# Kernel tuning notes

Hardware: AMD Instinct MI355X
Metric: run time of the kernel (lower is better)

The kernel has to match this reference:

```python
import jax, jax.numpy as jnp
import numpy as np

N = 50000        # nodes
E = 800000       # edges (avg degree 16)
F_IN = 128       # in_channels
HID = 32         # hidden_channels per head
H = 8            # heads
DH = HID * H     # 256, concat dim
NC = {'TL': 12, 'YL': 30, 'TS': 60, 'TZ': 120}
NEG_SLOPE = 0.2  # PyG GATConv default


def setup_inputs() -> dict:
    key = jax.random.key(0)
    ks = jax.random.split(key, 40)
    rn = lambda k, s, sc=0.1: jax.random.normal(k, s, jnp.float32) * sc
    inp = {}
    inp['x'] = jax.random.normal(ks[0], (N, F_IN), jnp.float32)
    inp['edge_index'] = jax.random.randint(ks[1], (2, E), 0, N, dtype=jnp.int64)
    # conv1: in -> H x HID (concat)
    inp['W1'] = rn(ks[2], (F_IN, DH)); inp['a1s'] = rn(ks[3], (H, HID)); inp['a1d'] = rn(ks[4], (H, HID)); inp['b1'] = jnp.zeros((DH,), jnp.float32)
    # conv2: DH -> H x HID (concat)
    inp['W2'] = rn(ks[5], (DH, DH)); inp['a2s'] = rn(ks[6], (H, HID)); inp['a2d'] = rn(ks[7], (H, HID)); inp['b2'] = jnp.zeros((DH,), jnp.float32)
    # task heads: DH -> C, heads=1, concat=False
    i = 8
    for t, c in NC.items():
        inp['W_' + t] = rn(ks[i], (DH, c)); i += 1
        inp['as_' + t] = rn(ks[i], (1, c)); i += 1
        inp['ad_' + t] = rn(ks[i], (1, c)); i += 1
        inp['b_' + t] = jnp.zeros((c,), jnp.float32)
    return inp


def gat_conv(x, src, dst, W, a_s, a_d, b, concat):
    """PyG-style GATConv (eval mode, self-loops already in src/dst)."""
    n = x.shape[0]
    heads, out_ch = a_s.shape
    h = (x @ W).reshape(n, heads, out_ch)                 # [N,H,C]
    alpha_s = jnp.einsum('nhc,hc->nh', h, a_s)            # [N,H]
    alpha_d = jnp.einsum('nhc,hc->nh', h, a_d)
    e = jax.nn.leaky_relu(alpha_s[src] + alpha_d[dst], NEG_SLOPE)   # [E,H]
    # numerically-stable segment softmax over incoming edges of each dst
    m = jax.ops.segment_max(e, dst, num_segments=n)
    ex = jnp.exp(e - m[dst])
    denom = jax.ops.segment_sum(ex, dst, num_segments=n)
    alpha = ex / (denom[dst] + 1e-16)                     # [E,H]
    out = jax.ops.segment_sum(alpha[:, :, None] * h[src], dst, num_segments=n)  # [N,H,C]
    out = out.reshape(n, heads * out_ch) if concat else out.mean(axis=1)
    return out + b


def reference(x, edge_index, W1, a1s, a1d, b1, W2, a2s, a2d, b2,
              W_TL, as_TL, ad_TL, b_TL, W_YL, as_YL, ad_YL, b_YL,
              W_TS, as_TS, ad_TS, b_TS, W_TZ, as_TZ, ad_TZ, b_TZ):
    n = x.shape[0]
    loop = jnp.arange(n, dtype=edge_index.dtype)
    src = jnp.concatenate([edge_index[0], loop])
    dst = jnp.concatenate([edge_index[1], loop])
    h = jax.nn.elu(gat_conv(x, src, dst, W1, a1s, a1d, b1, True))
    h = gat_conv(h, src, dst, W2, a2s, a2d, b2, True)
    tl = jax.nn.log_softmax(gat_conv(h, src, dst, W_TL, as_TL, ad_TL, b_TL, False), axis=1)
    yl = jax.nn.log_softmax(gat_conv(h, src, dst, W_YL, as_YL, ad_YL, b_YL, False), axis=1)
    ts = jax.nn.log_softmax(gat_conv(h, src, dst, W_TS, as_TS, ad_TS, b_TS, False), axis=1)
    tz = jax.nn.log_softmax(gat_conv(h, src, dst, W_TZ, as_TZ, ad_TZ, b_TZ, False), axis=1)
    return (tl, yl, ts, tz)
```

## Files before the change

### kernel.cpp

```cpp
#include <hip/hip_runtime.h>
#include <math.h>


#define NEG_SLOPE 0.2f

typedef short s8v __attribute__((ext_vector_type(8)));
typedef short s4v __attribute__((ext_vector_type(4)));
typedef float f4v __attribute__((ext_vector_type(4)));

__device__ __forceinline__ short f2bf(float x) {
    unsigned u = __float_as_uint(x);
    u += 0x7fffu + ((u >> 16) & 1u);
    return (short)(u >> 16);
}
__device__ __forceinline__ float bf2f(short b) {
    return __uint_as_float(((unsigned)(unsigned short)b) << 16);
}
__device__ __forceinline__ void split2(float x, short& h, short& l) {
    h = f2bf(x);
    l = f2bf(x - bf2f(h));
}
__device__ __forceinline__ float4 bf4_to_f4(s4v v) {
    return make_float4(bf2f(v[0]), bf2f(v[1]), bf2f(v[2]), bf2f(v[3]));
}
__device__ __forceinline__ int rfl_clamp(int v) {
    int s = __builtin_amdgcn_readfirstlane(v);
    return s < 0 ? 0 : s;
}


__global__ void init_kernel(int* __restrict__ deg, int* __restrict__ cursor, int n) {
    int i = blockIdx.x * blockDim.x + threadIdx.x;
    if (i < n) { deg[i] = 1; cursor[i] = 0; }
}

__global__ void count_kernel(const int* __restrict__ dst, int* __restrict__ deg, int E) {
    int i = blockIdx.x * blockDim.x + threadIdx.x;
    if (i < E) atomicAdd(&deg[dst[i]], 1);
}

__global__ __launch_bounds__(1024) void scan_kernel(const int* __restrict__ deg,
                                                    int* __restrict__ rowstart, int n) {
    __shared__ int wsum[16];
    __shared__ int carry_sh;
    int lane = threadIdx.x & 63, wv = threadIdx.x >> 6;
    if (threadIdx.x == 0) { carry_sh = 0; rowstart[0] = 0; }
    __syncthreads();
    for (int base = 0; base < n; base += 8192) {
        int vals[8];
        int sum = 0;
        int i0 = base + threadIdx.x * 8;
        #pragma unroll
        for (int j = 0; j < 8; ++j) {
            int i = i0 + j;
            int v = (i < n) ? ((deg[i] + 3) & ~3) : 0;
            sum += v;
            vals[j] = sum;
        }
        int incl = sum;
        #pragma unroll
        for (int off = 1; off < 64; off <<= 1) {
            int t = __shfl_up(incl, off);
            if (lane >= off) incl += t;
        }
        if (lane == 63) wsum[wv] = incl;
        __syncthreads();
        if (wv == 0) {
            int s = (lane < 16) ? wsum[lane] : 0;
            #pragma unroll
            for (int off = 1; off < 16; off <<= 1) {
                int t = __shfl_up(s, off);
                if (lane >= off) s += t;
            }
            if (lane < 16) wsum[lane] = s;
        }
        __syncthreads();
        int wexcl = (wv == 0) ? 0 : wsum[wv - 1];
        int excl = carry_sh + wexcl + (incl - sum);
        #pragma unroll
        for (int j = 0; j < 8; ++j) {
            int i = i0 + j;
            if (i < n) rowstart[i + 1] = excl + vals[j];
        }
        __syncthreads();
        if (threadIdx.x == 0) carry_sh += wsum[15];
        __syncthreads();
    }
}

__global__ void scatter_kernel(const int* __restrict__ src, const int* __restrict__ dst,
                               const int* __restrict__ rowstart, int* __restrict__ cursor,
                               int* __restrict__ csr, int* __restrict__ csrd, int E, int n) {
    int i = blockIdx.x * blockDim.x + threadIdx.x;
    if (i >= E + n) return;
    int s, d;
    if (i < E) { s = src[i]; d = dst[i]; }
    else       { s = d = i - E; }
    int p = atomicAdd(&cursor[d], 1);
    int slot = rowstart[d] + p;
    csr[slot] = s;
    csrd[slot] = d;
}


__global__ void tobf_kernel(const float* __restrict__ A, short* __restrict__ Ah, int n4) {
    int i = blockIdx.x * blockDim.x + threadIdx.x;
    if (i >= n4) return;
    float4 v = ((const float4*)A)[i];
    s4v hv = {f2bf(v.x), f2bf(v.y), f2bf(v.z), f2bf(v.w)};
    ((s4v*)Ah)[i] = hv;
}

__global__ void split_bt_kernel(const float* __restrict__ B, short* __restrict__ Bh,
                                short* __restrict__ Bl, int K, int Nc, int kshift) {
    int idx = blockIdx.x * blockDim.x + threadIdx.x;
    if (idx >= Nc * K) return;
    int n = idx >> kshift;
    int k = idx & (K - 1);
    float v = B[(size_t)k * Nc + n];
    short h, l; split2(v, h, l);
    Bh[idx] = h;
    Bl[idx] = l;
}

__global__ void fold_alpha8_kernel(const float* __restrict__ W,
                                   const float* __restrict__ a_s, const float* __restrict__ a_d,
                                   short* __restrict__ Bth, short* __restrict__ Btl,
                                   int K, int Nfeat) {
    int idx = blockIdx.x * blockDim.x + threadIdx.x;
    if (idx >= K * 16) return;
    int j = idx / K, k = idx % K;
    int h = j & 7;
    const float* av = ((j < 8) ? a_s : a_d) + h * 32;
    const float* wp = W + (size_t)k * 256 + h * 32;
    float s = 0.f;
    #pragma unroll
    for (int c = 0; c < 32; ++c) s += wp[c] * av[c];
    short hi, lo; split2(s, hi, lo);
    size_t off = (size_t)(Nfeat + j) * K + k;
    Bth[off] = hi; Btl[off] = lo;
}

__global__ void fold_alpha4_kernel(const float* __restrict__ Wcat,
                                   const float* __restrict__ ascat, const float* __restrict__ adcat,
                                   short* __restrict__ Bth, short* __restrict__ Btl) {
    int idx = blockIdx.x * blockDim.x + threadIdx.x;
    if (idx >= 256 * 8) return;
    int j = idx >> 8, k = idx & 255;
    const int CO[4] = {0, 12, 42, 102};
    const int CL[4] = {12, 30, 60, 120};
    int t = j & 3;
    const float* av = ((j < 4) ? ascat : adcat) + CO[t];
    const float* wp = Wcat + (size_t)k * 222 + CO[t];
    float s = 0.f;
    for (int c = 0; c < CL[t]; ++c) s += wp[c] * av[c];
    short hi, lo; split2(s, hi, lo);
    size_t off = (size_t)(222 + j) * 256 + k;
    Bth[off] = hi; Btl[off] = lo;
}


#define MB 128
#define NB 64
#define KS 32

__global__ __launch_bounds__(256) void gemm_mfma_kernel(
        const short* __restrict__ Ah_g,
        const short* __restrict__ Bth_g, const short* __restrict__ Btl_g,
        short* __restrict__ Cb, int cb_stride,
        float* __restrict__ als, float* __restrict__ ald, int nsplit,
        int M, int K, int Nfeat, int NcExt) {
    __shared__ __align__(16) short Ah[MB][40];
    __shared__ __align__(16) short Bh[NB][40];
    __shared__ __align__(16) short Bl[NB][40];

    int t = threadIdx.x;
    int lane = t & 63, w = t >> 6;
    int quad = lane >> 4, l16 = lane & 15;
    int row0 = blockIdx.y * MB, col0 = blockIdx.x * NB;

    f4v acc[2][4];
    #pragma unroll
    for (int mt = 0; mt < 2; ++mt)
        #pragma unroll
        for (int nt = 0; nt < 4; ++nt)
            acc[mt][nt] = (f4v){0.f, 0.f, 0.f, 0.f};

    for (int k0 = 0; k0 < K; k0 += KS) {
        __syncthreads();
        #pragma unroll
        for (int i = 0; i < 2; ++i) {
            int u = i * 256 + t;
            int r = u >> 2, kk = (u & 3) * 8;
            int gr = row0 + r;
            s8v vh = {0, 0, 0, 0, 0, 0, 0, 0};
            if (gr < M) vh = *(const s8v*)(Ah_g + (size_t)gr * K + k0 + kk);
            *(s8v*)&Ah[r][kk] = vh;
        }
        {
            int n = t >> 2, kk = (t & 3) * 8;
            int gc = col0 + n;
            s8v vh = {0, 0, 0, 0, 0, 0, 0, 0};
            s8v vl = {0, 0, 0, 0, 0, 0, 0, 0};
            if (gc < NcExt) {
                vh = *(const s8v*)(Bth_g + (size_t)gc * K + k0 + kk);
                vl = *(const s8v*)(Btl_g + (size_t)gc * K + k0 + kk);
            }
            *(s8v*)&Bh[n][kk] = vh;
            *(s8v*)&Bl[n][kk] = vl;
        }
        __syncthreads();

        int kb = quad * 8;
        s8v a_f[2], b_h[4], b_l[4];
        #pragma unroll
        for (int mt = 0; mt < 2; ++mt) {
            int r = w * 32 + mt * 16 + l16;
            a_f[mt] = *(const s8v*)&Ah[r][kb];
        }
        #pragma unroll
        for (int nt = 0; nt < 4; ++nt) {
            int c = nt * 16 + l16;
            b_h[nt] = *(const s8v*)&Bh[c][kb];
            b_l[nt] = *(const s8v*)&Bl[c][kb];
        }
        #pragma unroll
        for (int mt = 0; mt < 2; ++mt)
            #pragma unroll
            for (int nt = 0; nt < 4; ++nt) {
                acc[mt][nt] = __builtin_amdgcn_mfma_f32_16x16x32_bf16(
                    a_f[mt], b_h[nt], acc[mt][nt], 0, 0, 0);
                acc[mt][nt] = __builtin_amdgcn_mfma_f32_16x16x32_bf16(
                    a_f[mt], b_l[nt], acc[mt][nt], 0, 0, 0);
            }
    }

    #pragma unroll
    for (int mt = 0; mt < 2; ++mt) {
        #pragma unroll
        for (int nt = 0; nt < 4; ++nt) {
            int gc = col0 + nt * 16 + l16;
            if (gc >= NcExt) continue;
            #pragma unroll
            for (int r = 0; r < 4; ++r) {
                int gr = row0 + w * 32 + mt * 16 + quad * 4 + r;
                if (gr >= M) continue;
                float v = acc[mt][nt][r];
                if (gc < Nfeat) {
                    Cb[(size_t)gr * cb_stride + gc] = f2bf(v);
                } else {
                    int j = gc - Nfeat;
                    if (j < nsplit)            als[(size_t)gr * nsplit + j] = v;
                    else if (j < 2 * nsplit)   ald[(size_t)gr * nsplit + (j - nsplit)] = v;
                }
            }
        }
    }
}


__global__ void ew8_kernel(const float* __restrict__ als, const float* __restrict__ ald,
                           const int* __restrict__ csr, const int* __restrict__ csrd,
                           float* __restrict__ ew, int M4) {
    int i = blockIdx.x * blockDim.x + threadIdx.x;
    if (i >= M4) return;
    int s = csr[i], d = csrd[i];
    float4* op = (float4*)(ew + (size_t)i * 8);
    if (s < 0) {
        op[0] = make_float4(0.f, 0.f, 0.f, 0.f);
        op[1] = make_float4(0.f, 0.f, 0.f, 0.f);
        return;
    }
    const float4* ap = (const float4*)(als + (size_t)s * 8);
    const float4* dp = (const float4*)(ald + (size_t)d * 8);
    float4 a0 = ap[0], a1 = ap[1];
    float4 d0 = dp[0], d1 = dp[1];
    float v[8] = {a0.x + d0.x, a0.y + d0.y, a0.z + d0.z, a0.w + d0.w,
                  a1.x + d1.x, a1.y + d1.y, a1.z + d1.z, a1.w + d1.w};
    float w[8];
    #pragma unroll
    for (int h = 0; h < 8; ++h) {
        float x = v[h];
        x = (x > 0.f) ? x : NEG_SLOPE * x;
        w[h] = __expf(x);
    }
    op[0] = make_float4(w[0], w[1], w[2], w[3]);
    op[1] = make_float4(w[4], w[5], w[6], w[7]);
}


__global__ __launch_bounds__(256) void gat_gather_kernel(
        const short* __restrict__ hb, const float* __restrict__ ew,
        const int* __restrict__ rowstart, const int* __restrict__ csr,
        const float* __restrict__ bias, short* __restrict__ oh, int n, int elu) {
    int wid  = blockIdx.x * 4 + (threadIdx.x >> 6);
    int lane = threadIdx.x & 63;
    if (wid >= n) return;
    int row = rowstart[wid];
    int pdeg = rowstart[wid + 1] - row;
    int hp = lane >> 3;
    int ch = lane * 4;
    const int* cp = csr + row;
    const float* wp = ew + (size_t)row * 8 + hp;

    float4 acc = {0.f, 0.f, 0.f, 0.f};
    float wsum = 0.f;
    for (int e = 0; e < pdeg; e += 4) {
        int4 sv = *(const int4*)(cp + e);
        int s0 = rfl_clamp(sv.x);
        int s1 = rfl_clamp(sv.y);
        int s2 = rfl_clamp(sv.z);
        int s3 = rfl_clamp(sv.w);
        float w0 = wp[(size_t)(e + 0) * 8];
        float w1 = wp[(size_t)(e + 1) * 8];
        float w2 = wp[(size_t)(e + 2) * 8];
        float w3 = wp[(size_t)(e + 3) * 8];
        float4 h0 = bf4_to_f4(*(const s4v*)(hb + (size_t)s0 * 256 + ch));
        float4 h1 = bf4_to_f4(*(const s4v*)(hb + (size_t)s1 * 256 + ch));
        float4 h2 = bf4_to_f4(*(const s4v*)(hb + (size_t)s2 * 256 + ch));
        float4 h3 = bf4_to_f4(*(const s4v*)(hb + (size_t)s3 * 256 + ch));
        acc.x += w0 * h0.x + w1 * h1.x + w2 * h2.x + w3 * h3.x;
        acc.y += w0 * h0.y + w1 * h1.y + w2 * h2.y + w3 * h3.y;
        acc.z += w0 * h0.z + w1 * h1.z + w2 * h2.z + w3 * h3.z;
        acc.w += w0 * h0.w + w1 * h1.w + w2 * h2.w + w3 * h3.w;
        wsum += (w0 + w1) + (w2 + w3);
    }
    float inv = 1.f / (wsum + 1e-16f);
    float4 b4 = *(const float4*)(bias + ch);
    float v[4] = {acc.x * inv + b4.x, acc.y * inv + b4.y,
                  acc.z * inv + b4.z, acc.w * inv + b4.w};
    if (elu) {
        #pragma unroll
        for (int j = 0; j < 4; ++j)
            v[j] = (v[j] > 0.f) ? v[j] : __expf(v[j]) - 1.f;
    }
    s4v hv = {f2bf(v[0]), f2bf(v[1]), f2bf(v[2]), f2bf(v[3])};
    *(s4v*)(oh + (size_t)wid * 256 + ch) = hv;
}


__global__ void pack_w_kernel(const float* __restrict__ wTL, const float* __restrict__ wYL,
                              const float* __restrict__ wTS, const float* __restrict__ wTZ,
                              const float* __restrict__ bTL, const float* __restrict__ bYL,
                              const float* __restrict__ bTS, const float* __restrict__ bTZ,
                              const float* __restrict__ asTL, const float* __restrict__ asYL,
                              const float* __restrict__ asTS, const float* __restrict__ asTZ,
                              const float* __restrict__ adTL, const float* __restrict__ adYL,
                              const float* __restrict__ adTS, const float* __restrict__ adTZ,
                              float* __restrict__ Wcat, float* __restrict__ bcat,
                              float* __restrict__ ascat, float* __restrict__ adcat) {
    int idx = blockIdx.x * blockDim.x + threadIdx.x;
    if (idx < 256 * 222) {
        int r = idx / 222, c = idx % 222;
        float v;
        if (c < 12)       v = wTL[r * 12 + c];
        else if (c < 42)  v = wYL[r * 30 + (c - 12)];
        else if (c < 102) v = wTS[r * 60 + (c - 42)];
        else              v = wTZ[r * 120 + (c - 102)];
        Wcat[idx] = v;
    }
    if (idx < 222) {
        bcat[idx]  = (idx < 12) ? bTL[idx] : (idx < 42) ? bYL[idx - 12]
                   : (idx < 102) ? bTS[idx - 42] : bTZ[idx - 102];
        ascat[idx] = (idx < 12) ? asTL[idx] : (idx < 42) ? asYL[idx - 12]
                   : (idx < 102) ? asTS[idx - 42] : asTZ[idx - 102];
        adcat[idx] = (idx < 12) ? adTL[idx] : (idx < 42) ? adYL[idx - 12]
                   : (idx < 102) ? adTS[idx - 42] : adTZ[idx - 102];
    }
}


__global__ void ew4_kernel(const float* __restrict__ ast, const float* __restrict__ adt,
                           const int* __restrict__ csr, const int* __restrict__ csrd,
                           float* __restrict__ ew, int M4) {
    int i = blockIdx.x * blockDim.x + threadIdx.x;
    if (i >= M4) return;
    int s = csr[i], d = csrd[i];
    if (s < 0) {
        *(float4*)(ew + (size_t)i * 4) = make_float4(0.f, 0.f, 0.f, 0.f);
        return;
    }
    float4 a = *(const float4*)(ast + (size_t)s * 4);
    float4 b = *(const float4*)(adt + (size_t)d * 4);
    float v[4] = {a.x + b.x, a.y + b.y, a.z + b.z, a.w + b.w};
    float w[4];
    #pragma unroll
    for (int t = 0; t < 4; ++t) {
        float x = v[t];
        x = (x > 0.f) ? x : NEG_SLOPE * x;
        w[t] = __expf(x);
    }
    *(float4*)(ew + (size_t)i * 4) = make_float4(w[0], w[1], w[2], w[3]);
}


__device__ __forceinline__ float sel4(int t, float v0, float v1, float v2, float v3) {
    return (t == 0) ? v0 : (t == 1) ? v1 : (t == 2) ? v2 : v3;
}
__device__ __forceinline__ int sel4i(int t, int v0, int v1, int v2, int v3) {
    return (t == 0) ? v0 : (t == 1) ? v1 : (t == 2) ? v2 : v3;
}

__global__ __launch_bounds__(256) void task_gather_ls_kernel(
        const short* __restrict__ htb, const float* __restrict__ ew,
        const int* __restrict__ rowstart, const int* __restrict__ csr,
        const float* __restrict__ bcat, float* __restrict__ out, int n) {
    int wid  = blockIdx.x * 4 + (threadIdx.x >> 6);
    int lane = threadIdx.x & 63;
    if (wid >= n) return;
    int row = rowstart[wid];
    int pdeg = rowstart[wid + 1] - row;
    int ch0 = lane * 4;

    bool valj[4]; bool lo_j[4];
    int t_lo, t_hi;
    {
        int tj0 = (ch0 >= 102) ? 3 : (ch0 >= 42) ? 2 : (ch0 >= 12) ? 1 : 0;
        int ch3 = ch0 + 3;
        int tj3 = (ch3 >= 102) ? 3 : (ch3 >= 42) ? 2 : (ch3 >= 12) ? 1 : 0;
        t_lo = tj0; t_hi = tj3;
        #pragma unroll
        for (int j = 0; j < 4; ++j) {
            int ch = ch0 + j;
            valj[j] = (ch < 222);
            int tj = (ch >= 102) ? 3 : (ch >= 42) ? 2 : (ch >= 12) ? 1 : 0;
            lo_j[j] = (tj == t_lo);
        }
    }

    const int* cp = csr + row;
    const float* wp = ew + (size_t)row * 4;

    float acc[4] = {0.f, 0.f, 0.f, 0.f};
    float ws_lo = 0.f, ws_hi = 0.f;
    for (int e = 0; e < pdeg; e += 4) {
        int4 sv = *(const int4*)(cp + e);
        int s0 = rfl_clamp(sv.x);
        int s1 = rfl_clamp(sv.y);
        int s2 = rfl_clamp(sv.z);
        int s3 = rfl_clamp(sv.w);
        float wlo0 = wp[(size_t)(e + 0) * 4 + t_lo], whi0 = wp[(size_t)(e + 0) * 4 + t_hi];
        float wlo1 = wp[(size_t)(e + 1) * 4 + t_lo], whi1 = wp[(size_t)(e + 1) * 4 + t_hi];
        float wlo2 = wp[(size_t)(e + 2) * 4 + t_lo], whi2 = wp[(size_t)(e + 2) * 4 + t_hi];
        float wlo3 = wp[(size_t)(e + 3) * 4 + t_lo], whi3 = wp[(size_t)(e + 3) * 4 + t_hi];
        float4 h0 = bf4_to_f4(*(const s4v*)(htb + (size_t)s0 * 224 + ch0));
        float4 h1 = bf4_to_f4(*(const s4v*)(htb + (size_t)s1 * 224 + ch0));
        float4 h2 = bf4_to_f4(*(const s4v*)(htb + (size_t)s2 * 224 + ch0));
        float4 h3 = bf4_to_f4(*(const s4v*)(htb + (size_t)s3 * 224 + ch0));
        ws_lo += (wlo0 + wlo1) + (wlo2 + wlo3);
        ws_hi += (whi0 + whi1) + (whi2 + whi3);
        float hv0[4] = {h0.x, h0.y, h0.z, h0.w};
        float hv1[4] = {h1.x, h1.y, h1.z, h1.w};
        float hv2[4] = {h2.x, h2.y, h2.z, h2.w};
        float hv3[4] = {h3.x, h3.y, h3.z, h3.w};
        #pragma unroll
        for (int j = 0; j < 4; ++j) {
            float w0 = lo_j[j] ? wlo0 : whi0;
            float w1 = lo_j[j] ? wlo1 : whi1;
            float w2 = lo_j[j] ? wlo2 : whi2;
            float w3 = lo_j[j] ? wlo3 : whi3;
            acc[j] += w0 * hv0[j] + w1 * hv1[j] + w2 * hv2[j] + w3 * hv3[j];
        }
    }
    float inv_lo = 1.f / (ws_lo + 1e-16f);
    float inv_hi = 1.f / (ws_hi + 1e-16f);

    float vout[4];
    float m_lo = -1e30f, m_hi = -1e30f;
    #pragma unroll
    for (int j = 0; j < 4; ++j) {
        float v = 0.f;
        if (valj[j]) {
            v = acc[j] * (lo_j[j] ? inv_lo : inv_hi) + bcat[ch0 + j];
            if (lo_j[j]) m_lo = fmaxf(m_lo, v); else m_hi = fmaxf(m_hi, v);
        }
        vout[j] = v;
    }
    float m0 = -1e30f, m1 = -1e30f, m2 = -1e30f, m3 = -1e30f;
    m0 = (t_lo == 0) ? fmaxf(m0, m_lo) : m0;  m0 = (t_hi == 0) ? fmaxf(m0, m_hi) : m0;
    m1 = (t_lo == 1) ? fmaxf(m1, m_lo) : m1;  m1 = (t_hi == 1) ? fmaxf(m1, m_hi) : m1;
    m2 = (t_lo == 2) ? fmaxf(m2, m_lo) : m2;  m2 = (t_hi == 2) ? fmaxf(m2, m_hi) : m2;
    m3 = (t_lo == 3) ? fmaxf(m3, m_lo) : m3;  m3 = (t_hi == 3) ? fmaxf(m3, m_hi) : m3;
    #pragma unroll
    for (int off = 1; off < 64; off <<= 1) {
        m0 = fmaxf(m0, __shfl_xor(m0, off));
        m1 = fmaxf(m1, __shfl_xor(m1, off));
        m2 = fmaxf(m2, __shfl_xor(m2, off));
        m3 = fmaxf(m3, __shfl_xor(m3, off));
    }
    float mt_lo = sel4(t_lo, m0, m1, m2, m3);
    float mt_hi = sel4(t_hi, m0, m1, m2, m3);
    float s_lo = 0.f, s_hi = 0.f;
    #pragma unroll
    for (int j = 0; j < 4; ++j) {
        if (valj[j]) {
            if (lo_j[j]) s_lo += __expf(vout[j] - mt_lo);
            else         s_hi += __expf(vout[j] - mt_hi);
        }
    }
    float s0 = ((t_lo == 0) ? s_lo : 0.f) + ((t_hi == 0 && t_hi != t_lo) ? s_hi : 0.f);
    float s1 = ((t_lo == 1) ? s_lo : 0.f) + ((t_hi == 1 && t_hi != t_lo) ? s_hi : 0.f);
    float s2 = ((t_lo == 2) ? s_lo : 0.f) + ((t_hi == 2 && t_hi != t_lo) ? s_hi : 0.f);
    float s3 = ((t_lo == 3) ? s_lo : 0.f) + ((t_hi == 3 && t_hi != t_lo) ? s_hi : 0.f);
    #pragma unroll
    for (int off = 1; off < 64; off <<= 1) {
        s0 += __shfl_xor(s0, off);
        s1 += __shfl_xor(s1, off);
        s2 += __shfl_xor(s2, off);
        s3 += __shfl_xor(s3, off);
    }
    float l0 = m0 + __logf(s0), l1 = m1 + __logf(s1);
    float l2 = m2 + __logf(s2), l3 = m3 + __logf(s3);
    float lse_lo = sel4(t_lo, l0, l1, l2, l3);
    float lse_hi = sel4(t_hi, l0, l1, l2, l3);
    int co_lo = sel4i(t_lo, 0, 12, 42, 102), cl_lo = sel4i(t_lo, 12, 30, 60, 120);
    int co_hi = sel4i(t_hi, 0, 12, 42, 102), cl_hi = sel4i(t_hi, 12, 30, 60, 120);
    #pragma unroll
    for (int j = 0; j < 4; ++j) {
        if (!valj[j]) continue;
        int co = lo_j[j] ? co_lo : co_hi;
        int cl = lo_j[j] ? cl_lo : cl_hi;
        float lse = lo_j[j] ? lse_lo : lse_hi;
        out[(size_t)co * n + (size_t)wid * cl + (ch0 + j - co)] = vout[j] - lse;
    }
}


extern "C" void kernel_launch(void* const* d_in, const int* in_sizes, int n_in,
                              void* d_out, int out_size, void* d_ws, size_t ws_size,
                              hipStream_t stream) {
    const float* x   = (const float*)d_in[0];
    const int*   ei  = (const int*)d_in[1];
    const float* W1  = (const float*)d_in[2];
    const float* a1s = (const float*)d_in[3];
    const float* a1d = (const float*)d_in[4];
    const float* b1  = (const float*)d_in[5];
    const float* W2  = (const float*)d_in[6];
    const float* a2s = (const float*)d_in[7];
    const float* a2d = (const float*)d_in[8];
    const float* b2  = (const float*)d_in[9];
    const float* W_TL = (const float*)d_in[10]; const float* as_TL = (const float*)d_in[11];
    const float* ad_TL = (const float*)d_in[12]; const float* b_TL = (const float*)d_in[13];
    const float* W_YL = (const float*)d_in[14]; const float* as_YL = (const float*)d_in[15];
    const float* ad_YL = (const float*)d_in[16]; const float* b_YL = (const float*)d_in[17];
    const float* W_TS = (const float*)d_in[18]; const float* as_TS = (const float*)d_in[19];
    const float* ad_TS = (const float*)d_in[20]; const float* b_TS = (const float*)d_in[21];
    const float* W_TZ = (const float*)d_in[22]; const float* as_TZ = (const float*)d_in[23];
    const float* ad_TZ = (const float*)d_in[24]; const float* b_TZ = (const float*)d_in[25];

    const int N = in_sizes[0] / 128;
    const int E = in_sizes[1] / 2;
    const int* e_src = ei;
    const int* e_dst = ei + E;
    const int M4 = E + 4 * N;

    float* ws = (float*)d_ws;
    float* B1   = ws;
    float* B2   = B1 + (size_t)N * 256;
    float* B3   = B2 + (size_t)N * 256;
    float* as1  = B3 + (size_t)N * 256;
    float* ad1  = as1 + (size_t)N * 8;
    float* as2  = ad1 + (size_t)N * 8;
    float* ad2  = as2 + (size_t)N * 8;
    float* ast  = ad2 + (size_t)N * 8;
    float* adt  = ast + (size_t)N * 4;
    float* Wcat = adt + (size_t)N * 4;
    float* bcat = Wcat + 256 * 222;
    float* ascat = bcat + 224;
    float* adcat = ascat + 224;
    int* deg      = (int*)(adcat + 224);
    int* rowstart = deg + N;
    int* cursor   = rowstart + (N + 4);
    int* csr      = cursor + N;
    int* csrd     = csr + M4;
    uintptr_t wsp = (uintptr_t)(csrd + M4);
    wsp = (wsp + 15) & ~(uintptr_t)15;
    short* W1h = (short*)wsp;
    short* W1l = W1h + 272 * 128;
    short* W2h = W1l + 272 * 128;
    short* W2l = W2h + 272 * 256;
    short* Wth = W2l + 272 * 256;
    short* Wtl = Wth + 230 * 256;
    short* Xh  = (short*)B1;
    short* Sh  = (short*)B1;
    short* Th  = (short*)B1;
    short* h1b = (short*)B2;
    short* h2b = (short*)B2;
    short* htb = (short*)B2;
    float* ew1 = B3;
    float* ew2 = B3;
    float* ewt = B3;

    float* out = (float*)d_out;

    const int B = 256;
    init_kernel<<<(N + B - 1) / B, B, 0, stream>>>(deg, cursor, N);
    count_kernel<<<(E + B - 1) / B, B, 0, stream>>>(e_dst, deg, E);
    scan_kernel<<<1, 1024, 0, stream>>>(deg, rowstart, N);
    hipMemsetAsync(csr, 0xFF, (size_t)2 * M4 * sizeof(int), stream);
    scatter_kernel<<<(E + N + B - 1) / B, B, 0, stream>>>(e_src, e_dst, rowstart, cursor, csr, csrd, E, N);
    pack_w_kernel<<<(256 * 222 + B - 1) / B, B, 0, stream>>>(W_TL, W_YL, W_TS, W_TZ,
        b_TL, b_YL, b_TS, b_TZ, as_TL, as_YL, as_TS, as_TZ, ad_TL, ad_YL, ad_TS, ad_TZ,
        Wcat, bcat, ascat, adcat);
    split_bt_kernel<<<(256 * 128 + B - 1) / B, B, 0, stream>>>(W1, W1h, W1l, 128, 256, 7);
    split_bt_kernel<<<(256 * 256 + B - 1) / B, B, 0, stream>>>(W2, W2h, W2l, 256, 256, 8);
    split_bt_kernel<<<(222 * 256 + B - 1) / B, B, 0, stream>>>(Wcat, Wth, Wtl, 256, 222, 8);
    fold_alpha8_kernel<<<(128 * 16 + B - 1) / B, B, 0, stream>>>(W1, a1s, a1d, W1h, W1l, 128, 256);
    fold_alpha8_kernel<<<(256 * 16 + B - 1) / B, B, 0, stream>>>(W2, a2s, a2d, W2h, W2l, 256, 256);
    fold_alpha4_kernel<<<(256 * 8 + B - 1) / B, B, 0, stream>>>(Wcat, ascat, adcat, Wth, Wtl);
    tobf_kernel<<<((N * 128 / 4) + B - 1) / B, B, 0, stream>>>(x, Xh, N * 128 / 4);
    {
        dim3 g((272 + NB - 1) / NB, (N + MB - 1) / MB);
        gemm_mfma_kernel<<<g, 256, 0, stream>>>(Xh, W1h, W1l, h1b, 256,
                                                as1, ad1, 8, N, 128, 256, 272);
    }
    ew8_kernel<<<(M4 + B - 1) / B, B, 0, stream>>>(as1, ad1, csr, csrd, ew1, M4);
    gat_gather_kernel<<<(N + 3) / 4, 256, 0, stream>>>(h1b, ew1, rowstart, csr, b1, Sh, N, 1);
    {
        dim3 g((272 + NB - 1) / NB, (N + MB - 1) / MB);
        gemm_mfma_kernel<<<g, 256, 0, stream>>>(Sh, W2h, W2l, h2b, 256,
                                                as2, ad2, 8, N, 256, 256, 272);
    }
    ew8_kernel<<<(M4 + B - 1) / B, B, 0, stream>>>(as2, ad2, csr, csrd, ew2, M4);
    gat_gather_kernel<<<(N + 3) / 4, 256, 0, stream>>>(h2b, ew2, rowstart, csr, b2, Th, N, 0);
    {
        dim3 g((230 + NB - 1) / NB, (N + MB - 1) / MB);
        gemm_mfma_kernel<<<g, 256, 0, stream>>>(Th, Wth, Wtl, htb, 224,
                                                ast, adt, 4, N, 256, 222, 230);
    }
    ew4_kernel<<<(M4 + B - 1) / B, B, 0, stream>>>(ast, adt, csr, csrd, ewt, M4);
    task_gather_ls_kernel<<<(N + 3) / 4, 256, 0, stream>>>(htb, ewt, rowstart, csr, bcat, out, N);
}
```

Before: 631.3 us.

## Transpose edge weights to head-major, batch index loads via readlane in gathers

Edge attention weights are stored head-major ([H][M4]) instead of edge-major, so each lane reads contiguous float4 weights for a run of edges. The gather kernels load up to 64 CSR indices once per wave and broadcast them with readlane, unrolling by 8 to put more independent row loads in flight. The task-head columns are padded so each lane's 4 channels fall in a single task, which simplifies the log-softmax logic. The cost is strided writes in the ew kernels and slightly wider task GEMM output.

```diff
diff --git a/kernel.cpp b/kernel.cpp
--- a/kernel.cpp
+++ b/kernel.cpp
@@ -23,8 +23,8 @@
 __device__ __forceinline__ float4 bf4_to_f4(s4v v) {
     return make_float4(bf2f(v[0]), bf2f(v[1]), bf2f(v[2]), bf2f(v[3]));
 }
-__device__ __forceinline__ int rfl_clamp(int v) {
-    int s = __builtin_amdgcn_readfirstlane(v);
+__device__ __forceinline__ int rl_at(int v, int e) {
+    int s = __builtin_amdgcn_readlane(v, e);
     return s < 0 ? 0 : s;
 }
 
@@ -147,15 +147,15 @@
     int idx = blockIdx.x * blockDim.x + threadIdx.x;
     if (idx >= 256 * 8) return;
     int j = idx >> 8, k = idx & 255;
-    const int CO[4] = {0, 12, 42, 102};
-    const int CL[4] = {12, 30, 60, 120};
+    const int CO[4] = {0, 12, 44, 104};
+    const int CL[4] = {12, 32, 60, 120};
     int t = j & 3;
     const float* av = ((j < 4) ? ascat : adcat) + CO[t];
-    const float* wp = Wcat + (size_t)k * 222 + CO[t];
+    const float* wp = Wcat + (size_t)k * 224 + CO[t];
     float s = 0.f;
     for (int c = 0; c < CL[t]; ++c) s += wp[c] * av[c];
     short hi, lo; split2(s, hi, lo);
-    size_t off = (size_t)(222 + j) * 256 + k;
+    size_t off = (size_t)(224 + j) * 256 + k;
     Bth[off] = hi; Btl[off] = lo;
 }
 
@@ -261,14 +261,13 @@
 
 __global__ void ew8_kernel(const float* __restrict__ als, const float* __restrict__ ald,
                            const int* __restrict__ csr, const int* __restrict__ csrd,
-                           float* __restrict__ ew, int M4) {
+                           float* __restrict__ ewT, int M4) {
     int i = blockIdx.x * blockDim.x + threadIdx.x;
     if (i >= M4) return;
     int s = csr[i], d = csrd[i];
-    float4* op = (float4*)(ew + (size_t)i * 8);
     if (s < 0) {
-        op[0] = make_float4(0.f, 0.f, 0.f, 0.f);
-        op[1] = make_float4(0.f, 0.f, 0.f, 0.f);
+        #pragma unroll
+        for (int h = 0; h < 8; ++h) ewT[(size_t)h * M4 + i] = 0.f;
         return;
     }
     const float4* ap = (const float4*)(als + (size_t)s * 8);
@@ -277,22 +276,20 @@
     float4 d0 = dp[0], d1 = dp[1];
     float v[8] = {a0.x + d0.x, a0.y + d0.y, a0.z + d0.z, a0.w + d0.w,
                   a1.x + d1.x, a1.y + d1.y, a1.z + d1.z, a1.w + d1.w};
-    float w[8];
     #pragma unroll
     for (int h = 0; h < 8; ++h) {
         float x = v[h];
         x = (x > 0.f) ? x : NEG_SLOPE * x;
-        w[h] = __expf(x);
-    }
-    op[0] = make_float4(w[0], w[1], w[2], w[3]);
-    op[1] = make_float4(w[4], w[5], w[6], w[7]);
+        ewT[(size_t)h * M4 + i] = __expf(x);
+    }
 }
 
 
 __global__ __launch_bounds__(256) void gat_gather_kernel(
-        const short* __restrict__ hb, const float* __restrict__ ew,
+        const short* __restrict__ hb, const float* __restrict__ ewT,
         const int* __restrict__ rowstart, const int* __restrict__ csr,
-        const float* __restrict__ bias, short* __restrict__ oh, int n, int elu) {
+        const float* __restrict__ bias, short* __restrict__ oh, int n, int elu,
+        int M4) {
     int wid  = blockIdx.x * 4 + (threadIdx.x >> 6);
     int lane = threadIdx.x & 63;
     if (wid >= n) return;
@@ -301,29 +298,53 @@
     int hp = lane >> 3;
     int ch = lane * 4;
     const int* cp = csr + row;
-    const float* wp = ew + (size_t)row * 8 + hp;
+    const float* wp = ewT + (size_t)hp * M4 + row;
 
     float4 acc = {0.f, 0.f, 0.f, 0.f};
     float wsum = 0.f;
-    for (int e = 0; e < pdeg; e += 4) {
-        int4 sv = *(const int4*)(cp + e);
-        int s0 = rfl_clamp(sv.x);
-        int s1 = rfl_clamp(sv.y);
-        int s2 = rfl_clamp(sv.z);
-        int s3 = rfl_clamp(sv.w);
-        float w0 = wp[(size_t)(e + 0) * 8];
-        float w1 = wp[(size_t)(e + 1) * 8];
-        float w2 = wp[(size_t)(e + 2) * 8];
-        float w3 = wp[(size_t)(e + 3) * 8];
-        float4 h0 = bf4_to_f4(*(const s4v*)(hb + (size_t)s0 * 256 + ch));
-        float4 h1 = bf4_to_f4(*(const s4v*)(hb + (size_t)s1 * 256 + ch));
-        float4 h2 = bf4_to_f4(*(const s4v*)(hb + (size_t)s2 * 256 + ch));
-        float4 h3 = bf4_to_f4(*(const s4v*)(hb + (size_t)s3 * 256 + ch));
-        acc.x += w0 * h0.x + w1 * h1.x + w2 * h2.x + w3 * h3.x;
-        acc.y += w0 * h0.y + w1 * h1.y + w2 * h2.y + w3 * h3.y;
-        acc.z += w0 * h0.z + w1 * h1.z + w2 * h2.z + w3 * h3.z;
-        acc.w += w0 * h0.w + w1 * h1.w + w2 * h2.w + w3 * h3.w;
-        wsum += (w0 + w1) + (w2 + w3);
+    for (int base = 0; base < pdeg; base += 64) {
+        int cnt = min(pdeg - base, 64);
+        int idxv = -1;
+        if (lane < cnt) idxv = cp[base + lane];
+        const float* wpb = wp + base;
+        int e = 0;
+        for (; e + 8 <= cnt; e += 8) {
+            int si[8];
+            #pragma unroll
+            for (int i = 0; i < 8; ++i) si[i] = rl_at(idxv, e + i);
+            float4 wa = *(const float4*)(wpb + e);
+            float4 wb = *(const float4*)(wpb + e + 4);
+            s4v hv[8];
+            #pragma unroll
+            for (int i = 0; i < 8; ++i)
+                hv[i] = *(const s4v*)(hb + (size_t)si[i] * 256 + ch);
+            float wv[8] = {wa.x, wa.y, wa.z, wa.w, wb.x, wb.y, wb.z, wb.w};
+            #pragma unroll
+            for (int i = 0; i < 8; ++i) {
+                float4 h = bf4_to_f4(hv[i]);
+                acc.x += wv[i] * h.x; acc.y += wv[i] * h.y;
+                acc.z += wv[i] * h.z; acc.w += wv[i] * h.w;
+                wsum += wv[i];
+            }
+        }
+        for (; e < cnt; e += 4) {
+            int si[4];
+            #pragma unroll
+            for (int i = 0; i < 4; ++i) si[i] = rl_at(idxv, e + i);
+            float4 wa = *(const float4*)(wpb + e);
+            s4v hv[4];
+            #pragma unroll
+            for (int i = 0; i < 4; ++i)
+                hv[i] = *(const s4v*)(hb + (size_t)si[i] * 256 + ch);
+            float wv[4] = {wa.x, wa.y, wa.z, wa.w};
+            #pragma unroll
+            for (int i = 0; i < 4; ++i) {
+                float4 h = bf4_to_f4(hv[i]);
+                acc.x += wv[i] * h.x; acc.y += wv[i] * h.y;
+                acc.z += wv[i] * h.z; acc.w += wv[i] * h.w;
+                wsum += wv[i];
+            }
+        }
     }
     float inv = 1.f / (wsum + 1e-16f);
     float4 b4 = *(const float4*)(bias + ch);
@@ -334,8 +355,8 @@
         for (int j = 0; j < 4; ++j)
             v[j] = (v[j] > 0.f) ? v[j] : __expf(v[j]) - 1.f;
     }
-    s4v hv = {f2bf(v[0]), f2bf(v[1]), f2bf(v[2]), f2bf(v[3])};
-    *(s4v*)(oh + (size_t)wid * 256 + ch) = hv;
+    s4v hvo = {f2bf(v[0]), f2bf(v[1]), f2bf(v[2]), f2bf(v[3])};
+    *(s4v*)(oh + (size_t)wid * 256 + ch) = hvo;
 }
 
 
@@ -350,137 +371,139 @@
                               float* __restrict__ Wcat, float* __restrict__ bcat,
                               float* __restrict__ ascat, float* __restrict__ adcat) {
     int idx = blockIdx.x * blockDim.x + threadIdx.x;
-    if (idx < 256 * 222) {
-        int r = idx / 222, c = idx % 222;
-        float v;
+    if (idx < 256 * 224) {
+        int r = idx / 224, c = idx % 224;
+        float v = 0.f;
         if (c < 12)       v = wTL[r * 12 + c];
         else if (c < 42)  v = wYL[r * 30 + (c - 12)];
-        else if (c < 102) v = wTS[r * 60 + (c - 42)];
-        else              v = wTZ[r * 120 + (c - 102)];
+        else if (c < 44)  v = 0.f;
+        else if (c < 104) v = wTS[r * 60 + (c - 44)];
+        else              v = wTZ[r * 120 + (c - 104)];
         Wcat[idx] = v;
     }
-    if (idx < 222) {
-        bcat[idx]  = (idx < 12) ? bTL[idx] : (idx < 42) ? bYL[idx - 12]
-                   : (idx < 102) ? bTS[idx - 42] : bTZ[idx - 102];
-        ascat[idx] = (idx < 12) ? asTL[idx] : (idx < 42) ? asYL[idx - 12]
-                   : (idx < 102) ? asTS[idx - 42] : asTZ[idx - 102];
-        adcat[idx] = (idx < 12) ? adTL[idx] : (idx < 42) ? adYL[idx - 12]
-                   : (idx < 102) ? adTS[idx - 42] : adTZ[idx - 102];
+    if (idx < 224) {
+        float b = 0.f, as_ = 0.f, ad_ = 0.f;
+        if (idx < 12)       { b = bTL[idx];       as_ = asTL[idx];       ad_ = adTL[idx]; }
+        else if (idx < 42)  { b = bYL[idx - 12];  as_ = asYL[idx - 12];  ad_ = adYL[idx - 12]; }
+        else if (idx < 44)  { }
+        else if (idx < 104) { b = bTS[idx - 44];  as_ = asTS[idx - 44];  ad_ = adTS[idx - 44]; }
+        else                { b = bTZ[idx - 104]; as_ = asTZ[idx - 104]; ad_ = adTZ[idx - 104]; }
+        bcat[idx]  = b;
+        ascat[idx] = as_;
+        adcat[idx] = ad_;
     }
 }
 
 
 __global__ void ew4_kernel(const float* __restrict__ ast, const float* __restrict__ adt,
                            const int* __restrict__ csr, const int* __restrict__ csrd,
-                           float* __restrict__ ew, int M4) {
+                           float* __restrict__ ewT, int M4) {
     int i = blockIdx.x * blockDim.x + threadIdx.x;
     if (i >= M4) return;
     int s = csr[i], d = csrd[i];
     if (s < 0) {
-        *(float4*)(ew + (size_t)i * 4) = make_float4(0.f, 0.f, 0.f, 0.f);
+        #pragma unroll
+        for (int t = 0; t < 4; ++t) ewT[(size_t)t * M4 + i] = 0.f;
         return;
     }
     float4 a = *(const float4*)(ast + (size_t)s * 4);
     float4 b = *(const float4*)(adt + (size_t)d * 4);
     float v[4] = {a.x + b.x, a.y + b.y, a.z + b.z, a.w + b.w};
-    float w[4];
     #pragma unroll
     for (int t = 0; t < 4; ++t) {
         float x = v[t];
         x = (x > 0.f) ? x : NEG_SLOPE * x;
-        w[t] = __expf(x);
-    }
-    *(float4*)(ew + (size_t)i * 4) = make_float4(w[0], w[1], w[2], w[3]);
+        ewT[(size_t)t * M4 + i] = __expf(x);
+    }
 }
 
 
 __device__ __forceinline__ float sel4(int t, float v0, float v1, float v2, float v3) {
     return (t == 0) ? v0 : (t == 1) ? v1 : (t == 2) ? v2 : v3;
 }
-__device__ __forceinline__ int sel4i(int t, int v0, int v1, int v2, int v3) {
-    return (t == 0) ? v0 : (t == 1) ? v1 : (t == 2) ? v2 : v3;
-}
 
 __global__ __launch_bounds__(256) void task_gather_ls_kernel(
-        const short* __restrict__ htb, const float* __restrict__ ew,
+        const short* __restrict__ htb, const float* __restrict__ ewT,
         const int* __restrict__ rowstart, const int* __restrict__ csr,
-        const float* __restrict__ bcat, float* __restrict__ out, int n) {
+        const float* __restrict__ bcat, float* __restrict__ out, int n, int M4) {
     int wid  = blockIdx.x * 4 + (threadIdx.x >> 6);
     int lane = threadIdx.x & 63;
     if (wid >= n) return;
     int row = rowstart[wid];
     int pdeg = rowstart[wid + 1] - row;
     int ch0 = lane * 4;
-
-    bool valj[4]; bool lo_j[4];
-    int t_lo, t_hi;
-    {
-        int tj0 = (ch0 >= 102) ? 3 : (ch0 >= 42) ? 2 : (ch0 >= 12) ? 1 : 0;
-        int ch3 = ch0 + 3;
-        int tj3 = (ch3 >= 102) ? 3 : (ch3 >= 42) ? 2 : (ch3 >= 12) ? 1 : 0;
-        t_lo = tj0; t_hi = tj3;
-        #pragma unroll
-        for (int j = 0; j < 4; ++j) {
-            int ch = ch0 + j;
-            valj[j] = (ch < 222);
-            int tj = (ch >= 102) ? 3 : (ch >= 42) ? 2 : (ch >= 12) ? 1 : 0;
-            lo_j[j] = (tj == t_lo);
-        }
-    }
+    int t = (lane < 3) ? 0 : (lane < 11) ? 1 : (lane < 26) ? 2 : 3;
+    int COp = (t == 0) ? 0 : (t == 1) ? 12 : (t == 2) ? 44 : 104;
+    int COr = (t == 0) ? 0 : (t == 1) ? 12 : (t == 2) ? 42 : 102;
+    int CLr = (t == 0) ? 12 : (t == 1) ? 30 : (t == 2) ? 60 : 120;
+    bool valj[4];
+    #pragma unroll
+    for (int j = 0; j < 4; ++j)
+        valj[j] = (unsigned)(ch0 + j - COp) < (unsigned)CLr;
 
     const int* cp = csr + row;
-    const float* wp = ew + (size_t)row * 4;
+    const float* wp = ewT + (size_t)t * M4 + row;
 
     float acc[4] = {0.f, 0.f, 0.f, 0.f};
-    float ws_lo = 0.f, ws_hi = 0.f;
-    for (int e = 0; e < pdeg; e += 4) {
-        int4 sv = *(const int4*)(cp + e);
-        int s0 = rfl_clamp(sv.x);
-        int s1 = rfl_clamp(sv.y);
-        int s2 = rfl_clamp(sv.z);
-        int s3 = rfl_clamp(sv.w);
-        float wlo0 = wp[(size_t)(e + 0) * 4 + t_lo], whi0 = wp[(size_t)(e + 0) * 4 + t_hi];
-        float wlo1 = wp[(size_t)(e + 1) * 4 + t_lo], whi1 = wp[(size_t)(e + 1) * 4 + t_hi];
-        float wlo2 = wp[(size_t)(e + 2) * 4 + t_lo], whi2 = wp[(size_t)(e + 2) * 4 + t_hi];
-        float wlo3 = wp[(size_t)(e + 3) * 4 + t_lo], whi3 = wp[(size_t)(e + 3) * 4 + t_hi];
-        float4 h0 = bf4_to_f4(*(const s4v*)(htb + (size_t)s0 * 224 + ch0));
-        float4 h1 = bf4_to_f4(*(const s4v*)(htb + (size_t)s1 * 224 + ch0));
-        float4 h2 = bf4_to_f4(*(const s4v*)(htb + (size_t)s2 * 224 + ch0));
-        float4 h3 = bf4_to_f4(*(const s4v*)(htb + (size_t)s3 * 224 + ch0));
-        ws_lo += (wlo0 + wlo1) + (wlo2 + wlo3);
-        ws_hi += (whi0 + whi1) + (whi2 + whi3);
-        float hv0[4] = {h0.x, h0.y, h0.z, h0.w};
-        float hv1[4] = {h1.x, h1.y, h1.z, h1.w};
-        float hv2[4] = {h2.x, h2.y, h2.z, h2.w};
-        float hv3[4] = {h3.x, h3.y, h3.z, h3.w};
-        #pragma unroll
-        for (int j = 0; j < 4; ++j) {
-            float w0 = lo_j[j] ? wlo0 : whi0;
-            float w1 = lo_j[j] ? wlo1 : whi1;
-            float w2 = lo_j[j] ? wlo2 : whi2;
-            float w3 = lo_j[j] ? wlo3 : whi3;
-            acc[j] += w0 * hv0[j] + w1 * hv1[j] + w2 * hv2[j] + w3 * hv3[j];
-        }
-    }
-    float inv_lo = 1.f / (ws_lo + 1e-16f);
-    float inv_hi = 1.f / (ws_hi + 1e-16f);
+    float ws = 0.f;
+    for (int base = 0; base < pdeg; base += 64) {
+        int cnt = min(pdeg - base, 64);
+        int idxv = -1;
+        if (lane < cnt) idxv = cp[base + lane];
+        const float* wpb = wp + base;
+        int e = 0;
+        for (; e + 8 <= cnt; e += 8) {
+            int si[8];
+            #pragma unroll
+            for (int i = 0; i < 8; ++i) si[i] = rl_at(idxv, e + i);
+            float4 wa = *(const float4*)(wpb + e);
+            float4 wb = *(const float4*)(wpb + e + 4);
+            s4v hv[8];
+            #pragma unroll
+            for (int i = 0; i < 8; ++i)
+                hv[i] = *(const s4v*)(htb + (size_t)si[i] * 224 + ch0);
+            float wv[8] = {wa.x, wa.y, wa.z, wa.w, wb.x, wb.y, wb.z, wb.w};
+            #pragma unroll
+            for (int i = 0; i < 8; ++i) {
+                float4 h = bf4_to_f4(hv[i]);
+                acc[0] += wv[i] * h.x; acc[1] += wv[i] * h.y;
+                acc[2] += wv[i] * h.z; acc[3] += wv[i] * h.w;
+                ws += wv[i];
+            }
+        }
+        for (; e < cnt; e += 4) {
+            int si[4];
+            #pragma unroll
+            for (int i = 0; i < 4; ++i) si[i] = rl_at(idxv, e + i);
+            float4 wa = *(const float4*)(wpb + e);
+            s4v hv[4];
+            #pragma unroll
+            for (int i = 0; i < 4; ++i)
+                hv[i] = *(const s4v*)(htb + (size_t)si[i] * 224 + ch0);
+            float wv[4] = {wa.x, wa.y, wa.z, wa.w};
+            #pragma unroll
+            for (int i = 0; i < 4; ++i) {
+                float4 h = bf4_to_f4(hv[i]);
+                acc[0] += wv[i] * h.x; acc[1] += wv[i] * h.y;
+                acc[2] += wv[i] * h.z; acc[3] += wv[i] * h.w;
+                ws += wv[i];
+            }
+        }
+    }
+    float inv = 1.f / (ws + 1e-16f);
 
     float vout[4];
-    float m_lo = -1e30f, m_hi = -1e30f;
+    float m = -1e30f;
     #pragma unroll
     for (int j = 0; j < 4; ++j) {
         float v = 0.f;
-        if (valj[j]) {
-            v = acc[j] * (lo_j[j] ? inv_lo : inv_hi) + bcat[ch0 + j];
-            if (lo_j[j]) m_lo = fmaxf(m_lo, v); else m_hi = fmaxf(m_hi, v);
-        }
+        if (valj[j]) { v = acc[j] * inv + bcat[ch0 + j]; m = fmaxf(m, v); }
         vout[j] = v;
     }
-    float m0 = -1e30f, m1 = -1e30f, m2 = -1e30f, m3 = -1e30f;
-    m0 = (t_lo == 0) ? fmaxf(m0, m_lo) : m0;  m0 = (t_hi == 0) ? fmaxf(m0, m_hi) : m0;
-    m1 = (t_lo == 1) ? fmaxf(m1, m_lo) : m1;  m1 = (t_hi == 1) ? fmaxf(m1, m_hi) : m1;
-    m2 = (t_lo == 2) ? fmaxf(m2, m_lo) : m2;  m2 = (t_hi == 2) ? fmaxf(m2, m_hi) : m2;
-    m3 = (t_lo == 3) ? fmaxf(m3, m_lo) : m3;  m3 = (t_hi == 3) ? fmaxf(m3, m_hi) : m3;
+    float m0 = (t == 0) ? m : -1e30f;
+    float m1 = (t == 1) ? m : -1e30f;
+    float m2 = (t == 2) ? m : -1e30f;
+    float m3 = (t == 3) ? m : -1e30f;
     #pragma unroll
     for (int off = 1; off < 64; off <<= 1) {
         m0 = fmaxf(m0, __shfl_xor(m0, off));
@@ -488,20 +511,15 @@
         m2 = fmaxf(m2, __shfl_xor(m2, off));
         m3 = fmaxf(m3, __shfl_xor(m3, off));
     }
-    float mt_lo = sel4(t_lo, m0, m1, m2, m3);
-    float mt_hi = sel4(t_hi, m0, m1, m2, m3);
-    float s_lo = 0.f, s_hi = 0.f;
-    #pragma unroll
-    for (int j = 0; j < 4; ++j) {
-        if (valj[j]) {
-            if (lo_j[j]) s_lo += __expf(vout[j] - mt_lo);
-            else         s_hi += __expf(vout[j] - mt_hi);
-        }
-    }
-    float s0 = ((t_lo == 0) ? s_lo : 0.f) + ((t_hi == 0 && t_hi != t_lo) ? s_hi : 0.f);
-    float s1 = ((t_lo == 1) ? s_lo : 0.f) + ((t_hi == 1 && t_hi != t_lo) ? s_hi : 0.f);
-    float s2 = ((t_lo == 2) ? s_lo : 0.f) + ((t_hi == 2 && t_hi != t_lo) ? s_hi : 0.f);
-    float s3 = ((t_lo == 3) ? s_lo : 0.f) + ((t_hi == 3 && t_hi != t_lo) ? s_hi : 0.f);
+    float mt = sel4(t, m0, m1, m2, m3);
+    float sacc = 0.f;
+    #pragma unroll
+    for (int j = 0; j < 4; ++j)
+        if (valj[j]) sacc += __expf(vout[j] - mt);
+    float s0 = (t == 0) ? sacc : 0.f;
+    float s1 = (t == 1) ? sacc : 0.f;
+    float s2 = (t == 2) ? sacc : 0.f;
+    float s3 = (t == 3) ? sacc : 0.f;
     #pragma unroll
     for (int off = 1; off < 64; off <<= 1) {
         s0 += __shfl_xor(s0, off);
@@ -509,20 +527,12 @@
         s2 += __shfl_xor(s2, off);
         s3 += __shfl_xor(s3, off);
     }
-    float l0 = m0 + __logf(s0), l1 = m1 + __logf(s1);
-    float l2 = m2 + __logf(s2), l3 = m3 + __logf(s3);
-    float lse_lo = sel4(t_lo, l0, l1, l2, l3);
-    float lse_hi = sel4(t_hi, l0, l1, l2, l3);
-    int co_lo = sel4i(t_lo, 0, 12, 42, 102), cl_lo = sel4i(t_lo, 12, 30, 60, 120);
-    int co_hi = sel4i(t_hi, 0, 12, 42, 102), cl_hi = sel4i(t_hi, 12, 30, 60, 120);
-    #pragma unroll
-    for (int j = 0; j < 4; ++j) {
-        if (!valj[j]) continue;
-        int co = lo_j[j] ? co_lo : co_hi;
-        int cl = lo_j[j] ? cl_lo : cl_hi;
-        float lse = lo_j[j] ? lse_lo : lse_hi;
-        out[(size_t)co * n + (size_t)wid * cl + (ch0 + j - co)] = vout[j] - lse;
-    }
+    float st = sel4(t, s0, s1, s2, s3);
+    float lse = mt + __logf(st);
+    #pragma unroll
+    for (int j = 0; j < 4; ++j)
+        if (valj[j])
+            out[(size_t)COr * n + (size_t)wid * CLr + (ch0 + j - COp)] = vout[j] - lse;
 }
 
 
@@ -565,7 +575,7 @@
     float* ast  = ad2 + (size_t)N * 8;
     float* adt  = ast + (size_t)N * 4;
     float* Wcat = adt + (size_t)N * 4;
-    float* bcat = Wcat + 256 * 222;
+    float* bcat = Wcat + 256 * 224;
     float* ascat = bcat + 224;
     float* adcat = ascat + 224;
     int* deg      = (int*)(adcat + 224);
@@ -580,7 +590,7 @@
     short* W2h = W1l + 272 * 128;
     short* W2l = W2h + 272 * 256;
     short* Wth = W2l + 272 * 256;
-    short* Wtl = Wth + 230 * 256;
+    short* Wtl = Wth + 232 * 256;
     short* Xh  = (short*)B1;
     short* Sh  = (short*)B1;
     short* Th  = (short*)B1;
@@ -599,12 +609,12 @@
     scan_kernel<<<1, 1024, 0, stream>>>(deg, rowstart, N);
     hipMemsetAsync(csr, 0xFF, (size_t)2 * M4 * sizeof(int), stream);
     scatter_kernel<<<(E + N + B - 1) / B, B, 0, stream>>>(e_src, e_dst, rowstart, cursor, csr, csrd, E, N);
-    pack_w_kernel<<<(256 * 222 + B - 1) / B, B, 0, stream>>>(W_TL, W_YL, W_TS, W_TZ,
+    pack_w_kernel<<<(256 * 224 + B - 1) / B, B, 0, stream>>>(W_TL, W_YL, W_TS, W_TZ,
         b_TL, b_YL, b_TS, b_TZ, as_TL, as_YL, as_TS, as_TZ, ad_TL, ad_YL, ad_TS, ad_TZ,
         Wcat, bcat, ascat, adcat);
     split_bt_kernel<<<(256 * 128 + B - 1) / B, B, 0, stream>>>(W1, W1h, W1l, 128, 256, 7);
     split_bt_kernel<<<(256 * 256 + B - 1) / B, B, 0, stream>>>(W2, W2h, W2l, 256, 256, 8);
-    split_bt_kernel<<<(222 * 256 + B - 1) / B, B, 0, stream>>>(Wcat, Wth, Wtl, 256, 222, 8);
+    split_bt_kernel<<<(224 * 256 + B - 1) / B, B, 0, stream>>>(Wcat, Wth, Wtl, 256, 224, 8);
     fold_alpha8_kernel<<<(128 * 16 + B - 1) / B, B, 0, stream>>>(W1, a1s, a1d, W1h, W1l, 128, 256);
     fold_alpha8_kernel<<<(256 * 16 + B - 1) / B, B, 0, stream>>>(W2, a2s, a2d, W2h, W2l, 256, 256);
     fold_alpha4_kernel<<<(256 * 8 + B - 1) / B, B, 0, stream>>>(Wcat, ascat, adcat, Wth, Wtl);
@@ -615,19 +625,19 @@
                                                 as1, ad1, 8, N, 128, 256, 272);
     }
     ew8_kernel<<<(M4 + B - 1) / B, B, 0, stream>>>(as1, ad1, csr, csrd, ew1, M4);
-    gat_gather_kernel<<<(N + 3) / 4, 256, 0, stream>>>(h1b, ew1, rowstart, csr, b1, Sh, N, 1);
+    gat_gather_kernel<<<(N + 3) / 4, 256, 0, stream>>>(h1b, ew1, rowstart, csr, b1, Sh, N, 1, M4);
     {
         dim3 g((272 + NB - 1) / NB, (N + MB - 1) / MB);
         gemm_mfma_kernel<<<g, 256, 0, stream>>>(Sh, W2h, W2l, h2b, 256,
                                                 as2, ad2, 8, N, 256, 256, 272);
     }
     ew8_kernel<<<(M4 + B - 1) / B, B, 0, stream>>>(as2, ad2, csr, csrd, ew2, M4);
-    gat_gather_kernel<<<(N + 3) / 4, 256, 0, stream>>>(h2b, ew2, rowstart, csr, b2, Th, N, 0);
+    gat_gather_kernel<<<(N + 3) / 4, 256, 0, stream>>>(h2b, ew2, rowstart, csr, b2, Th, N, 0, M4);
     {
-        dim3 g((230 + NB - 1) / NB, (N + MB - 1) / MB);
+        dim3 g((232 + NB - 1) / NB, (N + MB - 1) / MB);
         gemm_mfma_kernel<<<g, 256, 0, stream>>>(Th, Wth, Wtl, htb, 224,
-                                                ast, adt, 4, N, 256, 222, 230);
+                                                ast, adt, 4, N, 256, 224, 232);
     }
     ew4_kernel<<<(M4 + B - 1) / B, B, 0, stream>>>(ast, adt, csr, csrd, ewt, M4);
-    task_gather_ls_kernel<<<(N + 3) / 4, 256, 0, stream>>>(htb, ewt, rowstart, csr, bcat, out, N);
-}
+    task_gather_ls_kernel<<<(N + 3) / 4, 256, 0, stream>>>(htb, ewt, rowstart, csr, bcat, out, N, M4);
+}
```

Measured after the change: 618.1 us. 2.1% less time.
